# Kernel tuning notes

Measured on AMD Instinct MI355X. Metric: run time of the kernel, lower is better.

Reference implementation:

```python
import jax, jax.numpy as jnp
import numpy as np

B, T, D, V, L = 32, 512, 512, 1024, 128
BLANK = 0
NEG = -1e30  # log-domain 'minus infinity' that is fp-safe


def setup_inputs() -> dict:
    key = jax.random.key(0)
    k1, k2, k3 = jax.random.split(key, 3)
    x = jax.random.normal(k1, (B, T, D), dtype=jnp.float32)
    W = jax.random.normal(k2, (D, V), dtype=jnp.float32) / np.sqrt(D).astype(np.float32)
    b = jnp.zeros((V,), dtype=jnp.float32)
    # CTC targets must be in [1, V) (never the blank id 0)
    target = jax.random.randint(k3, (B, L), 1, V)
    input_lengths = jnp.full((B,), T, dtype=jnp.int32)
    target_lengths = jnp.full((B,), L, dtype=jnp.int32)
    return {"x": x, "W": W, "b": b, "target": target,
            "input_lengths": input_lengths, "target_lengths": target_lengths}


def _ctc_loss(log_probs, target, input_lengths, target_lengths):
    # log_probs: [T, B, V] (time-major), target: [B, L]
    Tt, Bb, _ = log_probs.shape
    Ll = target.shape[1]
    S = 2 * Ll + 1  # extended label sequence: blank,t0,blank,t1,...,blank
    ext = jnp.full((Bb, S), BLANK, dtype=target.dtype).at[:, 1::2].set(target)  # [B,S]
    ext_m2 = jnp.pad(ext, ((0, 0), (2, 0)), constant_values=BLANK)[:, :S]
    skip = (ext != BLANK) & (ext != ext_m2) & (jnp.arange(S)[None, :] >= 2)  # [B,S]

    # gather log-probs of extended labels for every time step: [T,B,S]
    lp_ext = jnp.take_along_axis(log_probs, jnp.broadcast_to(ext[None], (Tt, Bb, S)), axis=2)

    alpha0 = jnp.full((Bb, S), NEG, log_probs.dtype)
    alpha0 = alpha0.at[:, 0].set(lp_ext[0, :, 0]).at[:, 1].set(lp_ext[0, :, 1])

    def step(alpha, lp_t):
        a1 = jnp.pad(alpha, ((0, 0), (1, 0)), constant_values=NEG)[:, :S]
        a2 = jnp.pad(alpha, ((0, 0), (2, 0)), constant_values=NEG)[:, :S]
        c = jnp.logaddexp(alpha, a1)
        c = jnp.where(skip, jnp.logaddexp(c, a2), c)
        new = c + lp_t
        return new, new

    _, alphas = jax.lax.scan(step, alpha0, lp_ext[1:])
    alphas = jnp.concatenate([alpha0[None], alphas], axis=0)  # [T,B,S]

    bi = jnp.arange(Bb)
    a_last = alphas[input_lengths - 1, bi]  # [B,S] alpha at each sample's final frame
    ll = jnp.logaddexp(a_last[bi, 2 * target_lengths - 1], a_last[bi, 2 * target_lengths])
    nll = -ll  # per-sample negative log-likelihood
    # zero_infinity=True: infinite losses are zeroed
    nll = jnp.where(jnp.isinf(nll) | (nll > 1e29), 0.0, nll)
    # reduction='mean': divide each loss by its target length, then mean
    return jnp.mean(nll / jnp.maximum(target_lengths, 1).astype(nll.dtype))


def reference(x, W, b, target, input_lengths, target_lengths):
    logits = jnp.einsum('btd,dv->btv', x, W) + b  # nn.Linear
    log_probs = jax.nn.log_softmax(logits, axis=-1)  # [B,T,V]
    return _ctc_loss(jnp.transpose(log_probs, (1, 0, 2)), target, input_lengths, target_lengths)
```

## Files before the change

### kernel.cpp

```cpp
#include <hip/hip_runtime.h>
#include <cstdint>


#define SPAD 260
#define PEXT_PAD_ROWS 64
#define L2E 1.4426950408889634f
#define LN2 0.6931471805599453f

typedef short v8s __attribute__((ext_vector_type(8)));
typedef float v4f __attribute__((ext_vector_type(4)));

__device__ __forceinline__ uint32_t f2bf_bits(float f) {
  uint32_t u = __float_as_uint(f);
  return (u + 0x7FFFu + ((u >> 16) & 1u)) >> 16;
}
__device__ __forceinline__ float bf2f(uint32_t h) { return __uint_as_float(h << 16); }

__global__ void k_prep(const float* __restrict__ x, uint16_t* __restrict__ xb, long long n,
                       const float* __restrict__ W, uint16_t* __restrict__ Wt, int D, int V,
                       float* __restrict__ out, int nconv) {
  if (blockIdx.x == 0 && threadIdx.x == 0) out[0] = 0.f;
  if ((int)blockIdx.x < nconv) {
    long long i = ((long long)blockIdx.x * blockDim.x + threadIdx.x) * 8;
    if (i >= n) return;
    float4 a = *(const float4*)(x + i);
    float4 b = *(const float4*)(x + i + 4);
    uint4 o;
    o.x = f2bf_bits(a.x) | (f2bf_bits(a.y) << 16);
    o.y = f2bf_bits(a.z) | (f2bf_bits(a.w) << 16);
    o.z = f2bf_bits(b.x) | (f2bf_bits(b.y) << 16);
    o.w = f2bf_bits(b.z) | (f2bf_bits(b.w) << 16);
    *(uint4*)(xb + i) = o;
  } else {
    __shared__ float tile[32][33];
    const int bid2 = blockIdx.x - nconv;
    const int n0 = (bid2 % (V / 32)) * 32, k0 = (bid2 / (V / 32)) * 32;
    const int tx = threadIdx.x & 31, ty = threadIdx.x >> 5;
    #pragma unroll
    for (int i = 0; i < 32; i += 8)
      tile[ty + i][tx] = W[(size_t)(k0 + ty + i) * V + n0 + tx];
    __syncthreads();
    #pragma unroll
    for (int i = 0; i < 32; i += 8)
      Wt[(size_t)(n0 + ty + i) * D + k0 + tx] = (uint16_t)f2bf_bits(tile[tx][ty + i]);
  }
}

__global__ __launch_bounds__(256) void k_gemm(const uint16_t* __restrict__ A,
                                              const uint16_t* __restrict__ Bt,
                                              const float* __restrict__ bias,
                                              uint16_t* __restrict__ C, int M, int N, int K) {
  __shared__ uint16_t As[2][128 * 32];
  __shared__ uint16_t Bs[2][128 * 32];
  const int tid = threadIdx.x, lane = tid & 63, wave = tid >> 6;
  const int m0 = blockIdx.x * 128, n0 = blockIdx.y * 128;
  const int wm = wave & 1, wn = wave >> 1;
  const int frow = lane & 15, kb = lane >> 4;
  const int lr = lane >> 2, kc = lane & 3;
  v4f acc[4][4] = {};

  for (int k0 = 0; k0 < K; k0 += 64) {
    __syncthreads();
    #pragma unroll
    for (int t = 0; t < 2; t++)
      #pragma unroll
      for (int i = 0; i < 2; i++) {
        const int r = (wave * 2 + i) * 16 + lr;
        const uint16_t* ga = A + (size_t)(m0 + r) * K + k0 + t * 32 + kc * 8;
        const uint16_t* gb = Bt + (size_t)(n0 + r) * K + k0 + t * 32 + kc * 8;
        __builtin_amdgcn_global_load_lds(
            (const __attribute__((address_space(1))) void*)ga,
            (__attribute__((address_space(3))) void*)(&As[t][0] + (wave * 2 + i) * 512 + lane * 8), 16, 0, 0);
        __builtin_amdgcn_global_load_lds(
            (const __attribute__((address_space(1))) void*)gb,
            (__attribute__((address_space(3))) void*)(&Bs[t][0] + (wave * 2 + i) * 512 + lane * 8), 16, 0, 0);
      }
    __syncthreads();

    #pragma unroll
    for (int t = 0; t < 2; t++) {
      v8s af[4], bf[4];
      #pragma unroll
      for (int i = 0; i < 4; i++)
        af[i] = *(const v8s*)(&As[t][0] + (wm * 64 + i * 16 + frow) * 32 + kb * 8);
      #pragma unroll
      for (int j = 0; j < 4; j++)
        bf[j] = *(const v8s*)(&Bs[t][0] + (wn * 64 + j * 16 + frow) * 32 + kb * 8);
      #pragma unroll
      for (int i = 0; i < 4; i++)
        #pragma unroll
        for (int j = 0; j < 4; j++)
          acc[i][j] = __builtin_amdgcn_mfma_f32_16x16x32_bf16(af[i], bf[j], acc[i][j], 0, 0, 0);
    }
  }

  const int crow = (lane >> 4) * 4, ccol = lane & 15;
  #pragma unroll
  for (int j = 0; j < 4; j++) {
    const int n = n0 + wn * 64 + j * 16 + ccol;
    const float bv = bias[n];
    #pragma unroll
    for (int i = 0; i < 4; i++) {
      const int mb = m0 + wm * 64 + i * 16 + crow;
      #pragma unroll
      for (int r2 = 0; r2 < 4; r2++)
        C[(size_t)(mb + r2) * N + n] = (uint16_t)f2bf_bits(acc[i][j][r2] + bv);
    }
  }
}

__global__ void k_softmax_gather(const uint16_t* __restrict__ logits, const int* __restrict__ target,
                                 const int* __restrict__ tlen, float* __restrict__ pext,
                                 int T, int V, int L) {
  const int row = blockIdx.x * 4 + (threadIdx.x >> 6);
  const int lane = threadIdx.x & 63;
  const uint16_t* lrow = logits + (size_t)row * V;

  float xs[16];
  int cnt = 0;
  float mx = -INFINITY;
  for (int base = 0; base < V; base += 256) {
    const int idx = base + lane * 4;
    uint2 u = *(const uint2*)(lrow + idx);
    float4 v;
    v.x = bf2f(u.x & 0xFFFFu); v.y = bf2f(u.x >> 16);
    v.z = bf2f(u.y & 0xFFFFu); v.w = bf2f(u.y >> 16);
    xs[cnt] = v.x; xs[cnt + 1] = v.y; xs[cnt + 2] = v.z; xs[cnt + 3] = v.w; cnt += 4;
    mx = fmaxf(mx, fmaxf(fmaxf(v.x, v.y), fmaxf(v.z, v.w)));
  }
  #pragma unroll
  for (int off = 32; off; off >>= 1) mx = fmaxf(mx, __shfl_xor(mx, off, 64));
  float sum = 0.f;
  #pragma unroll
  for (int q = 0; q < 16; q++) { if (q < cnt) sum += exp2f((xs[q] - mx) * L2E); }
  #pragma unroll
  for (int off = 32; off; off >>= 1) sum += __shfl_xor(sum, off, 64);
  const float lse2 = mx * L2E + log2f(sum);

  const int bidx = row / T;
  const int Lb = tlen[bidx];
  const int S = 2 * Lb + 1;
  float* prow = pext + (size_t)row * SPAD;
  for (int s = lane; s < SPAD; s += 64) {
    float p = 0.f;
    if (s < S) {
      const int lbl = (s & 1) ? target[bidx * L + ((s - 1) >> 1)] : 0;
      p = exp2f(bf2f(lrow[lbl]) * L2E - lse2);
    }
    prow[s] = p;
  }
}

__device__ __forceinline__ float wave_shr1(float x) {
  return __int_as_float(__builtin_amdgcn_update_dpp(0, __float_as_int(x), 0x138, 0xf, 0xf, true));
}
__device__ __forceinline__ float wave_max_nonneg(float x) {
  x = fmaxf(x, __int_as_float(__builtin_amdgcn_update_dpp(0, __float_as_int(x), 0x111, 0xf, 0xf, true)));
  x = fmaxf(x, __int_as_float(__builtin_amdgcn_update_dpp(0, __float_as_int(x), 0x112, 0xf, 0xf, true)));
  x = fmaxf(x, __int_as_float(__builtin_amdgcn_update_dpp(0, __float_as_int(x), 0x114, 0xf, 0xf, true)));
  x = fmaxf(x, __int_as_float(__builtin_amdgcn_update_dpp(0, __float_as_int(x), 0x118, 0xf, 0xf, true)));
  x = fmaxf(x, __int_as_float(__builtin_amdgcn_update_dpp(0, __float_as_int(x), 0x142, 0xf, 0xf, true)));
  x = fmaxf(x, __int_as_float(__builtin_amdgcn_update_dpp(0, __float_as_int(x), 0x143, 0xf, 0xf, true)));
  return __int_as_float(__builtin_amdgcn_readlane(__float_as_int(x), 63));
}

__device__ __forceinline__ void load8(float4* __restrict__ p, float* __restrict__ p4,
                                      const float* __restrict__ pb, int t0, int lane) {
  #pragma unroll
  for (int k = 0; k < 8; k++) {
    const float* row = pb + (size_t)(t0 + k) * SPAD;
    p[k] = *(const float4*)(row + (lane << 2));
    p4[k] = row[256];
  }
}

__global__ __launch_bounds__(64, 1) void k_ctc(const float* __restrict__ pext,
                                               const int* __restrict__ target,
                                               const int* __restrict__ ilen,
                                               const int* __restrict__ tlen,
                                               float* __restrict__ out, int T, int L) {
  const int b = blockIdx.x;
  const int lane = threadIdx.x;
  const int B = gridDim.x;
  const int Tb = ilen[b];
  const int Lb = tlen[b];
  const int S = 2 * Lb + 1;
  const int* tg = target + b * L;

  const int s1 = 4 * lane + 1, s3 = 4 * lane + 3;
  float sk1 = 0.f, sk3 = 0.f;
  if (s1 >= 3 && s1 < S) sk1 = (tg[(s1 - 1) >> 1] != tg[(s1 - 3) >> 1]) ? 1.f : 0.f;
  if (s3 >= 3 && s3 < S) sk3 = (tg[(s3 - 1) >> 1] != tg[(s3 - 3) >> 1]) ? 1.f : 0.f;

  const float* pb = pext + (size_t)b * T * SPAD;
  const float4 p0 = *(const float4*)(pb + (lane << 2));
  float a0 = (lane == 0) ? p0.x : 0.f;
  float a1 = (lane == 0) ? p0.y : 0.f;
  float a2 = 0.f, a3 = 0.f, a4 = 0.f;
  float log2C = 0.f;

  #define CTC_STEP(PP, P4) {                                            \
    const float pm3 = wave_shr1(a3);                                    \
    const float a255 = __int_as_float(__builtin_amdgcn_readlane(__float_as_int(a3), 63)); \
    const float n0v = (a0 + pm3) * (PP).x;                              \
    const float n1v = (a1 + a0 + sk1 * pm3) * (PP).y;                   \
    const float n2v = (a2 + a1) * (PP).z;                               \
    const float n3v = (a3 + a2 + sk3 * a1) * (PP).w;                    \
    const float n4v = (a4 + a255) * (P4);                               \
    a0 = n0v; a1 = n1v; a2 = n2v; a3 = n3v; a4 = n4v; }

  #define RENORM {                                                      \
    float m = fmaxf(fmaxf(fmaxf(a0, a1), fmaxf(a2, a3)), a4);           \
    m = wave_max_nonneg(m);                                             \
    const int e = (int)((__float_as_uint(m) >> 23) & 255u) - 127;       \
    const float scale = __uint_as_float((uint32_t)(127 - e) << 23);     \
    a0 *= scale; a1 *= scale; a2 *= scale; a3 *= scale; a4 *= scale;    \
    log2C += (float)e; }

  float4 Pa[8], Pb_[8], Pc[8], Pd[8];
  float Qa[8], Qb[8], Qc[8], Qd[8];
  int t0 = 1;
  bool done = false;
  load8(Pa, Qa, pb, t0, lane);
  load8(Pb_, Qb, pb, t0 + 8, lane);
  load8(Pc, Qc, pb, t0 + 16, lane);
  __builtin_amdgcn_sched_barrier(0);

  #define PHASE(LP, LQ, CP, CQ) {                                       \
    if (t0 + 8 <= Tb) {                                                 \
      load8(LP, LQ, pb, t0 + 24, lane);                                 \
      __builtin_amdgcn_sched_barrier(0);                                \
      _Pragma("unroll")                                                 \
      for (int k = 0; k < 8; k++) CTC_STEP(CP[k], CQ[k]);               \
      RENORM; t0 += 8;                                                  \
    } else {                                                            \
      _Pragma("unroll")                                                 \
      for (int k = 0; k < 8; k++) { if (t0 + k < Tb) CTC_STEP(CP[k], CQ[k]); } \
      RENORM; done = true;                                              \
    } }

  while (!done) {
    PHASE(Pd, Qd, Pa, Qa); if (done) break;
    PHASE(Pa, Qa, Pb_, Qb); if (done) break;
    PHASE(Pb_, Qb, Pc, Qc); if (done) break;
    PHASE(Pc, Qc, Pd, Qd);
  }

  __shared__ float abuf[257];
  abuf[4 * lane + 0] = a0; abuf[4 * lane + 1] = a1;
  abuf[4 * lane + 2] = a2; abuf[4 * lane + 3] = a3;
  if (lane == 63) abuf[256] = a4;
  __syncthreads();
  if (lane == 0) {
    const float ssum = abuf[2 * Lb - 1] + abuf[2 * Lb];
    const float ll = (log2f(ssum) + log2C) * LN2;
    float nll = -ll;
    if (!(nll < 1e29f)) nll = 0.f;
    atomicAdd(out, nll / ((float)(Lb > 0 ? Lb : 1) * (float)B));
  }
}

extern "C" void kernel_launch(void* const* d_in, const int* in_sizes, int n_in,
                              void* d_out, int out_size, void* d_ws, size_t ws_size,
                              hipStream_t stream) {
  const float* x      = (const float*)d_in[0];
  const float* W      = (const float*)d_in[1];
  const float* bias   = (const float*)d_in[2];
  const int*  target  = (const int*)d_in[3];
  const int*  ilen    = (const int*)d_in[4];
  const int*  tlen    = (const int*)d_in[5];

  const int B = in_sizes[4];
  const int V = in_sizes[2];
  const int D = in_sizes[1] / V;
  const int T = in_sizes[0] / (B * D);
  const int L = in_sizes[3] / B;
  const int M = B * T;

  char* ws = (char*)d_ws;
  const size_t xb_bytes = (size_t)M * D * 2;
  const size_t wt_bytes = (size_t)V * D * 2;
  const size_t pext_bytes = (size_t)(M + PEXT_PAD_ROWS) * SPAD * 4;
  uint16_t* xb = (uint16_t*)ws;
  uint16_t* Wt = (uint16_t*)(ws + xb_bytes);
  uint16_t* logits = (uint16_t*)(ws + xb_bytes + wt_bytes);
  const size_t log_bytes = (size_t)M * V * 2;

  float* pext;
  if (pext_bytes <= xb_bytes + wt_bytes) {
    pext = (float*)ws;
  } else {
    pext = (float*)(ws + xb_bytes + wt_bytes + log_bytes);
  }

  const long long nx = (long long)M * D;
  const int nconv = (int)((nx / 8 + 255) / 256);
  const int ntrans = (V / 32) * (D / 32);
  k_prep<<<nconv + ntrans, 256, 0, stream>>>(x, xb, nx, W, Wt, D, V, (float*)d_out, nconv);
  k_gemm<<<dim3(M / 128, V / 128), 256, 0, stream>>>(xb, Wt, bias, logits, M, V, D);
  k_softmax_gather<<<M / 4, 256, 0, stream>>>(logits, target, tlen, pext, T, V, L);
  k_ctc<<<B, 64, 0, stream>>>(pext, target, ilen, tlen, (float*)d_out, T, L);
}
```

Measured before the change: 167.3 us.

## Stream CTC probabilities through an LDS ring via async global-to-LDS loads

The CTC recurrence kernel now prefetches 8-timestep chunks into an 8-slot shared-memory ring using global_load_lds, issued six chunks ahead with explicit vmcnt waits. This replaces the register-held quad buffers and hides global latency on the serial critical path. The 257th state column moves to a separate compact array that is staged into LDS once. The GEMM also gets a 1D grid with an XCD-aware block remap, and the pext row stride drops to 256. The risks are the hardcoded vmcnt(48) counting, and the p4 staging being capped at 1024 timesteps.

```diff
diff --git a/kernel.cpp b/kernel.cpp
--- a/kernel.cpp
+++ b/kernel.cpp
@@ -2,8 +2,10 @@
 #include <cstdint>
 
 
-#define SPAD 260
+#define PROW 256
 #define PEXT_PAD_ROWS 64
+#define CTC_D 6
+#define CTC_NS 8
 #define L2E 1.4426950408889634f
 #define LN2 0.6931471805599453f
 
@@ -53,7 +55,11 @@
   __shared__ uint16_t As[2][128 * 32];
   __shared__ uint16_t Bs[2][128 * 32];
   const int tid = threadIdx.x, lane = tid & 63, wave = tid >> 6;
-  const int m0 = blockIdx.x * 128, n0 = blockIdx.y * 128;
+  int d = blockIdx.x;
+  const int nwg = gridDim.x;
+  if ((nwg & 7) == 0) d = (d & 7) * (nwg >> 3) + (d >> 3);
+  const int ntl = N >> 7;
+  const int m0 = (d / ntl) * 128, n0 = (d % ntl) * 128;
   const int wm = wave & 1, wn = wave >> 1;
   const int frow = lane & 15, kb = lane >> 4;
   const int lr = lane >> 2, kc = lane & 3;
@@ -111,7 +117,7 @@
 
 __global__ void k_softmax_gather(const uint16_t* __restrict__ logits, const int* __restrict__ target,
                                  const int* __restrict__ tlen, float* __restrict__ pext,
-                                 int T, int V, int L) {
+                                 float* __restrict__ p4arr, int T, int V, int L) {
   const int row = blockIdx.x * 4 + (threadIdx.x >> 6);
   const int lane = threadIdx.x & 63;
   const uint16_t* lrow = logits + (size_t)row * V;
@@ -140,14 +146,21 @@
   const int bidx = row / T;
   const int Lb = tlen[bidx];
   const int S = 2 * Lb + 1;
-  float* prow = pext + (size_t)row * SPAD;
-  for (int s = lane; s < SPAD; s += 64) {
+  float* prow = pext + (size_t)row * PROW;
+  #pragma unroll
+  for (int it = 0; it < PROW / 64; it++) {
+    const int s = lane + it * 64;
     float p = 0.f;
     if (s < S) {
       const int lbl = (s & 1) ? target[bidx * L + ((s - 1) >> 1)] : 0;
       p = exp2f(bf2f(lrow[lbl]) * L2E - lse2);
     }
     prow[s] = p;
+  }
+  if (lane == 0) {
+    float p = 0.f;
+    if (256 < S) p = exp2f(bf2f(lrow[0]) * L2E - lse2);
+    p4arr[row] = p;
   }
 }
 
@@ -164,21 +177,16 @@
   return __int_as_float(__builtin_amdgcn_readlane(__float_as_int(x), 63));
 }
 
-__device__ __forceinline__ void load8(float4* __restrict__ p, float* __restrict__ p4,
-                                      const float* __restrict__ pb, int t0, int lane) {
-  #pragma unroll
-  for (int k = 0; k < 8; k++) {
-    const float* row = pb + (size_t)(t0 + k) * SPAD;
-    p[k] = *(const float4*)(row + (lane << 2));
-    p4[k] = row[256];
-  }
-}
-
 __global__ __launch_bounds__(64, 1) void k_ctc(const float* __restrict__ pext,
+                                               const float* __restrict__ p4arr,
                                                const int* __restrict__ target,
                                                const int* __restrict__ ilen,
                                                const int* __restrict__ tlen,
                                                float* __restrict__ out, int T, int L) {
+  __shared__ __attribute__((aligned(16))) float ring[CTC_NS][8][PROW];
+  __shared__ float p4l[1024 + 8];
+  __shared__ float abuf[257];
+
   const int b = blockIdx.x;
   const int lane = threadIdx.x;
   const int B = gridDim.x;
@@ -192,12 +200,31 @@
   if (s1 >= 3 && s1 < S) sk1 = (tg[(s1 - 1) >> 1] != tg[(s1 - 3) >> 1]) ? 1.f : 0.f;
   if (s3 >= 3 && s3 < S) sk3 = (tg[(s3 - 1) >> 1] != tg[(s3 - 3) >> 1]) ? 1.f : 0.f;
 
-  const float* pb = pext + (size_t)b * T * SPAD;
+  const float* pb = pext + (size_t)b * T * PROW;
+  const float* p4b = p4arr + (size_t)b * T;
+
   const float4 p0 = *(const float4*)(pb + (lane << 2));
   float a0 = (lane == 0) ? p0.x : 0.f;
   float a1 = (lane == 0) ? p0.y : 0.f;
   float a2 = 0.f, a3 = 0.f, a4 = 0.f;
   float log2C = 0.f;
+
+  int ng = (T + 63) >> 6; if (ng > 16) ng = 16;
+  for (int g = 0; g < ng; g++)
+    __builtin_amdgcn_global_load_lds(
+        (const __attribute__((address_space(1))) void*)(p4b + g * 64 + lane),
+        (__attribute__((address_space(3))) void*)(&p4l[g * 64]), 4, 0, 0);
+
+  const int CT = (Tb + 6) >> 3;
+
+  #define ISSUE(c) {                                                        \
+    const int _slot = (c) & (CTC_NS - 1);                                   \
+    const float* _src = pb + (size_t)(1 + 8 * (c)) * PROW + (lane << 2);    \
+    _Pragma("unroll")                                                       \
+    for (int _k = 0; _k < 8; _k++)                                          \
+      __builtin_amdgcn_global_load_lds(                                     \
+          (const __attribute__((address_space(1))) void*)(_src + _k * PROW),\
+          (__attribute__((address_space(3))) void*)(&ring[_slot][_k][0]), 16, 0, 0); }
 
   #define CTC_STEP(PP, P4) {                                            \
     const float pm3 = wave_shr1(a3);                                    \
@@ -217,36 +244,35 @@
     a0 *= scale; a1 *= scale; a2 *= scale; a3 *= scale; a4 *= scale;    \
     log2C += (float)e; }
 
-  float4 Pa[8], Pb_[8], Pc[8], Pd[8];
-  float Qa[8], Qb[8], Qc[8], Qd[8];
-  int t0 = 1;
-  bool done = false;
-  load8(Pa, Qa, pb, t0, lane);
-  load8(Pb_, Qb, pb, t0 + 8, lane);
-  load8(Pc, Qc, pb, t0 + 16, lane);
-  __builtin_amdgcn_sched_barrier(0);
-
-  #define PHASE(LP, LQ, CP, CQ) {                                       \
-    if (t0 + 8 <= Tb) {                                                 \
-      load8(LP, LQ, pb, t0 + 24, lane);                                 \
-      __builtin_amdgcn_sched_barrier(0);                                \
-      _Pragma("unroll")                                                 \
-      for (int k = 0; k < 8; k++) CTC_STEP(CP[k], CQ[k]);               \
-      RENORM; t0 += 8;                                                  \
-    } else {                                                            \
-      _Pragma("unroll")                                                 \
-      for (int k = 0; k < 8; k++) { if (t0 + k < Tb) CTC_STEP(CP[k], CQ[k]); } \
-      RENORM; done = true;                                              \
-    } }
-
-  while (!done) {
-    PHASE(Pd, Qd, Pa, Qa); if (done) break;
-    PHASE(Pa, Qa, Pb_, Qb); if (done) break;
-    PHASE(Pb_, Qb, Pc, Qc); if (done) break;
-    PHASE(Pc, Qc, Pd, Qd);
-  }
-
-  __shared__ float abuf[257];
+  const int npre = CT < CTC_D ? CT : CTC_D;
+  for (int c = 0; c < npre; c++) ISSUE(c);
+
+  for (int c = 0; c < CT; c++) {
+    if (c + CTC_D < CT) {
+      ISSUE(c + CTC_D);
+      asm volatile("s_waitcnt vmcnt(48)" ::: "memory");
+    } else {
+      asm volatile("s_waitcnt vmcnt(0)" ::: "memory");
+    }
+    const int slot = c & (CTC_NS - 1);
+    const int t0 = 1 + 8 * c;
+    float4 P[8]; float Q[8];
+    #pragma unroll
+    for (int k = 0; k < 8; k++) {
+      P[k] = *(const float4*)(&ring[slot][k][lane << 2]);
+      Q[k] = p4l[t0 + k];
+    }
+    if (t0 + 8 <= Tb) {
+      #pragma unroll
+      for (int k = 0; k < 8; k++) CTC_STEP(P[k], Q[k]);
+      RENORM;
+    } else {
+      #pragma unroll
+      for (int k = 0; k < 8; k++) { if (t0 + k < Tb) CTC_STEP(P[k], Q[k]); }
+      RENORM;
+    }
+  }
+
   abuf[4 * lane + 0] = a0; abuf[4 * lane + 1] = a1;
   abuf[4 * lane + 2] = a2; abuf[4 * lane + 3] = a3;
   if (lane == 63) abuf[256] = a4;
@@ -280,24 +306,27 @@
   char* ws = (char*)d_ws;
   const size_t xb_bytes = (size_t)M * D * 2;
   const size_t wt_bytes = (size_t)V * D * 2;
-  const size_t pext_bytes = (size_t)(M + PEXT_PAD_ROWS) * SPAD * 4;
   uint16_t* xb = (uint16_t*)ws;
   uint16_t* Wt = (uint16_t*)(ws + xb_bytes);
   uint16_t* logits = (uint16_t*)(ws + xb_bytes + wt_bytes);
   const size_t log_bytes = (size_t)M * V * 2;
 
-  float* pext;
-  if (pext_bytes <= xb_bytes + wt_bytes) {
+  const size_t pext_bytes = (size_t)(M + PEXT_PAD_ROWS) * PROW * 4;
+  const size_t p4_bytes = (size_t)(M + PEXT_PAD_ROWS) * 4;
+  float* pext; float* p4a;
+  if (pext_bytes + p4_bytes <= xb_bytes + wt_bytes) {
     pext = (float*)ws;
+    p4a  = (float*)(ws + pext_bytes);
   } else {
     pext = (float*)(ws + xb_bytes + wt_bytes + log_bytes);
+    p4a  = (float*)(ws + xb_bytes + wt_bytes + log_bytes + pext_bytes);
   }
 
   const long long nx = (long long)M * D;
   const int nconv = (int)((nx / 8 + 255) / 256);
   const int ntrans = (V / 32) * (D / 32);
   k_prep<<<nconv + ntrans, 256, 0, stream>>>(x, xb, nx, W, Wt, D, V, (float*)d_out, nconv);
-  k_gemm<<<dim3(M / 128, V / 128), 256, 0, stream>>>(xb, Wt, bias, logits, M, V, D);
-  k_softmax_gather<<<M / 4, 256, 0, stream>>>(logits, target, tlen, pext, T, V, L);
-  k_ctc<<<B, 64, 0, stream>>>(pext, target, ilen, tlen, (float*)d_out, T, L);
-}
+  k_gemm<<<(M / 128) * (V / 128), 256, 0, stream>>>(xb, Wt, bias, logits, M, V, D);
+  k_softmax_gather<<<M / 4, 256, 0, stream>>>(logits, target, tlen, pext, p4a, T, V, L);
+  k_ctc<<<B, 64, 0, stream>>>(pext, p4a, target, ilen, tlen, (float*)d_out, T, L);
+}
```

Result: slower. 175.7 us (+5.0%).

## Shrink pext rows to 256 floats and remap GEMM blocks across XCDs

Applied to the files above, without the earlier changes.

The CTC probability row width drops from 260 to 256 floats. The final extended position (a blank) takes its value from lane 0's blank probability through a readlane, since every blank slot holds the same probability. This removes one extra scalar load per time step in the serial CTC recurrence and gives 1 KB-aligned rows. Separately, the GEMM now launches on a 1D grid and swizzles block IDs so consecutive tiles land on the same XCD, aiming for better L2 reuse of shared A/B tiles.

```diff
diff --git a/kernel.cpp b/kernel.cpp
--- a/kernel.cpp
+++ b/kernel.cpp
@@ -2,7 +2,7 @@
 #include <cstdint>
 
 
-#define SPAD 260
+#define PROW 256
 #define PEXT_PAD_ROWS 64
 #define L2E 1.4426950408889634f
 #define LN2 0.6931471805599453f
@@ -53,7 +53,11 @@
   __shared__ uint16_t As[2][128 * 32];
   __shared__ uint16_t Bs[2][128 * 32];
   const int tid = threadIdx.x, lane = tid & 63, wave = tid >> 6;
-  const int m0 = blockIdx.x * 128, n0 = blockIdx.y * 128;
+  int d = blockIdx.x;
+  const int nwg = gridDim.x;
+  if ((nwg & 7) == 0) d = (d & 7) * (nwg >> 3) + (d >> 3);
+  const int ntl = N >> 7;
+  const int m0 = (d / ntl) * 128, n0 = (d % ntl) * 128;
   const int wm = wave & 1, wn = wave >> 1;
   const int frow = lane & 15, kb = lane >> 4;
   const int lr = lane >> 2, kc = lane & 3;
@@ -140,8 +144,10 @@
   const int bidx = row / T;
   const int Lb = tlen[bidx];
   const int S = 2 * Lb + 1;
-  float* prow = pext + (size_t)row * SPAD;
-  for (int s = lane; s < SPAD; s += 64) {
+  float* prow = pext + (size_t)row * PROW;
+  #pragma unroll
+  for (int it = 0; it < PROW / 64; it++) {
+    const int s = lane + it * 64;
     float p = 0.f;
     if (s < S) {
       const int lbl = (s & 1) ? target[bidx * L + ((s - 1) >> 1)] : 0;
@@ -164,14 +170,11 @@
   return __int_as_float(__builtin_amdgcn_readlane(__float_as_int(x), 63));
 }
 
-__device__ __forceinline__ void load8(float4* __restrict__ p, float* __restrict__ p4,
+__device__ __forceinline__ void load8(float4* __restrict__ p,
                                       const float* __restrict__ pb, int t0, int lane) {
   #pragma unroll
-  for (int k = 0; k < 8; k++) {
-    const float* row = pb + (size_t)(t0 + k) * SPAD;
-    p[k] = *(const float4*)(row + (lane << 2));
-    p4[k] = row[256];
-  }
+  for (int k = 0; k < 8; k++)
+    p[k] = *(const float4*)(pb + (size_t)(t0 + k) * PROW + (lane << 2));
 }
 
 __global__ __launch_bounds__(64, 1) void k_ctc(const float* __restrict__ pext,
@@ -192,21 +195,22 @@
   if (s1 >= 3 && s1 < S) sk1 = (tg[(s1 - 1) >> 1] != tg[(s1 - 3) >> 1]) ? 1.f : 0.f;
   if (s3 >= 3 && s3 < S) sk3 = (tg[(s3 - 1) >> 1] != tg[(s3 - 3) >> 1]) ? 1.f : 0.f;
 
-  const float* pb = pext + (size_t)b * T * SPAD;
+  const float* pb = pext + (size_t)b * T * PROW;
   const float4 p0 = *(const float4*)(pb + (lane << 2));
   float a0 = (lane == 0) ? p0.x : 0.f;
   float a1 = (lane == 0) ? p0.y : 0.f;
   float a2 = 0.f, a3 = 0.f, a4 = 0.f;
   float log2C = 0.f;
 
-  #define CTC_STEP(PP, P4) {                                            \
+  #define CTC_STEP(PP) {                                                \
     const float pm3 = wave_shr1(a3);                                    \
     const float a255 = __int_as_float(__builtin_amdgcn_readlane(__float_as_int(a3), 63)); \
+    const float p4v = __int_as_float(__builtin_amdgcn_readlane(__float_as_int((PP).x), 0)); \
     const float n0v = (a0 + pm3) * (PP).x;                              \
     const float n1v = (a1 + a0 + sk1 * pm3) * (PP).y;                   \
     const float n2v = (a2 + a1) * (PP).z;                               \
     const float n3v = (a3 + a2 + sk3 * a1) * (PP).w;                    \
-    const float n4v = (a4 + a255) * (P4);                               \
+    const float n4v = (a4 + a255) * p4v;                                \
     a0 = n0v; a1 = n1v; a2 = n2v; a3 = n3v; a4 = n4v; }
 
   #define RENORM {                                                      \
@@ -218,32 +222,31 @@
     log2C += (float)e; }
 
   float4 Pa[8], Pb_[8], Pc[8], Pd[8];
-  float Qa[8], Qb[8], Qc[8], Qd[8];
   int t0 = 1;
   bool done = false;
-  load8(Pa, Qa, pb, t0, lane);
-  load8(Pb_, Qb, pb, t0 + 8, lane);
-  load8(Pc, Qc, pb, t0 + 16, lane);
+  load8(Pa, pb, t0, lane);
+  load8(Pb_, pb, t0 + 8, lane);
+  load8(Pc, pb, t0 + 16, lane);
   __builtin_amdgcn_sched_barrier(0);
 
-  #define PHASE(LP, LQ, CP, CQ) {                                       \
+  #define PHASE(LP, CP) {                                               \
     if (t0 + 8 <= Tb) {                                                 \
-      load8(LP, LQ, pb, t0 + 24, lane);                                 \
+      load8(LP, pb, t0 + 24, lane);                                     \
       __builtin_amdgcn_sched_barrier(0);                                \
       _Pragma("unroll")                                                 \
-      for (int k = 0; k < 8; k++) CTC_STEP(CP[k], CQ[k]);               \
+      for (int k = 0; k < 8; k++) CTC_STEP(CP[k]);                      \
       RENORM; t0 += 8;                                                  \
     } else {                                                            \
       _Pragma("unroll")                                                 \
-      for (int k = 0; k < 8; k++) { if (t0 + k < Tb) CTC_STEP(CP[k], CQ[k]); } \
+      for (int k = 0; k < 8; k++) { if (t0 + k < Tb) CTC_STEP(CP[k]); } \
       RENORM; done = true;                                              \
     } }
 
   while (!done) {
-    PHASE(Pd, Qd, Pa, Qa); if (done) break;
-    PHASE(Pa, Qa, Pb_, Qb); if (done) break;
-    PHASE(Pb_, Qb, Pc, Qc); if (done) break;
-    PHASE(Pc, Qc, Pd, Qd);
+    PHASE(Pd, Pa); if (done) break;
+    PHASE(Pa, Pb_); if (done) break;
+    PHASE(Pb_, Pc); if (done) break;
+    PHASE(Pc, Pd);
   }
 
   __shared__ float abuf[257];
@@ -280,12 +283,12 @@
   char* ws = (char*)d_ws;
   const size_t xb_bytes = (size_t)M * D * 2;
   const size_t wt_bytes = (size_t)V * D * 2;
-  const size_t pext_bytes = (size_t)(M + PEXT_PAD_ROWS) * SPAD * 4;
   uint16_t* xb = (uint16_t*)ws;
   uint16_t* Wt = (uint16_t*)(ws + xb_bytes);
   uint16_t* logits = (uint16_t*)(ws + xb_bytes + wt_bytes);
   const size_t log_bytes = (size_t)M * V * 2;
 
+  const size_t pext_bytes = (size_t)(M + PEXT_PAD_ROWS) * PROW * 4;
   float* pext;
   if (pext_bytes <= xb_bytes + wt_bytes) {
     pext = (float*)ws;
@@ -297,7 +300,7 @@
   const int nconv = (int)((nx / 8 + 255) / 256);
   const int ntrans = (V / 32) * (D / 32);
   k_prep<<<nconv + ntrans, 256, 0, stream>>>(x, xb, nx, W, Wt, D, V, (float*)d_out, nconv);
-  k_gemm<<<dim3(M / 128, V / 128), 256, 0, stream>>>(xb, Wt, bias, logits, M, V, D);
+  k_gemm<<<(M / 128) * (V / 128), 256, 0, stream>>>(xb, Wt, bias, logits, M, V, D);
   k_softmax_gather<<<M / 4, 256, 0, stream>>>(logits, target, tlen, pext, T, V, L);
   k_ctc<<<B, 64, 0, stream>>>(pext, target, ilen, tlen, (float*)d_out, T, L);
 }
```

Result: faster. 160.2 us (-4.3%).
